# Kernel tuning notes

Hardware: AMD Instinct MI355X
Metric: run time of the kernel (lower is better)

The kernel has to match this reference:

```python
import jax, jax.numpy as jnp
import numpy as np

N = 100000      # nodes
E = 1600000     # edges (before self-loops)
IN_DIM = 128
HID = 32
HEADS = 4
OUT_DIM = 64
NEG_SLOPE = 0.2  # PyG GATConv default


def setup_inputs() -> dict:
    key = jax.random.key(0)
    ks = jax.random.split(key, 12)
    s1 = 1.0 / np.sqrt(IN_DIM).astype(np.float32)
    s2 = 1.0 / np.sqrt(HEADS * HID).astype(np.float32)
    return {
        "x": jax.random.normal(ks[0], (N, IN_DIM), jnp.float32),
        "edge_index": jax.random.randint(ks[1], (2, E), 0, N, dtype=jnp.int64),
        "W1": jax.random.normal(ks[2], (IN_DIM, HEADS * HID), jnp.float32) * s1,
        "att_src1": jax.random.normal(ks[3], (HEADS, HID), jnp.float32) * 0.1,
        "att_dst1": jax.random.normal(ks[4], (HEADS, HID), jnp.float32) * 0.1,
        "b1": jnp.zeros((HEADS * HID,), jnp.float32),
        "W2": jax.random.normal(ks[5], (HEADS * HID, OUT_DIM), jnp.float32) * s2,
        "att_src2": jax.random.normal(ks[6], (1, OUT_DIM), jnp.float32) * 0.1,
        "att_dst2": jax.random.normal(ks[7], (1, OUT_DIM), jnp.float32) * 0.1,
        "b2": jnp.zeros((OUT_DIM,), jnp.float32),
    }


def _gat_layer(x, src, dst, W, att_src, att_dst, bias, heads, out_ch, concat):
    # x: [N, F_in] -> h: [N, H, C]
    n = x.shape[0]
    h = (x @ W).reshape(n, heads, out_ch)
    # per-node attention logits, [N, H]
    a_src = jnp.einsum("nhc,hc->nh", h, att_src)
    a_dst = jnp.einsum("nhc,hc->nh", h, att_dst)
    # edge logits + LeakyReLU, [E, H]
    e = a_src[src] + a_dst[dst]
    e = jnp.where(e >= 0, e, NEG_SLOPE * e)
    # segment softmax over incoming edges of each dst node
    m = jax.ops.segment_max(e, dst, num_segments=n)          # [N, H]
    e = jnp.exp(e - m[dst])
    denom = jax.ops.segment_sum(e, dst, num_segments=n)      # [N, H]
    alpha = e / (denom[dst] + 1e-16)                          # [E, H]
    # weighted scatter-aggregate of source messages -> [N, H, C]
    out = jax.ops.segment_sum(h[src] * alpha[:, :, None], dst, num_segments=n)
    if concat:
        out = out.reshape(n, heads * out_ch)
    else:
        out = out.mean(axis=1)
    return out + bias


def reference(x, edge_index, W1, att_src1, att_dst1, b1, W2, att_src2, att_dst2, b2):
    n = x.shape[0]
    # PyG GATConv adds self-loops by default
    loops = jnp.arange(n, dtype=edge_index.dtype)
    src = jnp.concatenate([edge_index[0], loops])
    dst = jnp.concatenate([edge_index[1], loops])
    h = _gat_layer(x, src, dst, W1, att_src1, att_dst1, b1, HEADS, HID, concat=True)
    h = jax.nn.elu(h)
    # dropout p=0.5 is identity in eval mode (training=False)
    out = _gat_layer(h, src, dst, W2, att_src2, att_dst2, b2, 1, OUT_DIM, concat=False)
    return out
```

## Files before the change

### kernel.cpp

```cpp
#include <hip/hip_runtime.h>
#include <hip/hip_bf16.h>
#include <hip/hip_fp16.h>

#define NEG 0.2f
#define L2E 1.44269504f
#define BSH 9
#define BNODES 512
#define MAXC 16384
#define CHUNK 4096

typedef __attribute__((ext_vector_type(8))) _Float16 half8v;
typedef __attribute__((ext_vector_type(4))) short short4v;
typedef __attribute__((ext_vector_type(4))) float f32x4;

__device__ __forceinline__ float leaky(float e) { return fmaxf(e, NEG * e); }
__device__ __forceinline__ ushort f2h(float f) {
    __half h = __float2half(f);
    return *reinterpret_cast<ushort*>(&h);
}
__device__ __forceinline__ float edgep(float l, float adv, float e0) {
    return __builtin_amdgcn_exp2f(leaky(l + adv) - e0);
}

__device__ __forceinline__ void fma8(float* acc, float a, uint4 h) {
    unsigned wv[4] = { h.x, h.y, h.z, h.w };
    #pragma unroll
    for (int j = 0; j < 4; j++) {
        __half2 hh = *reinterpret_cast<__half2*>(&wv[j]);
        float lo = __half2float(__low2half(hh));
        float hi = __half2float(__high2half(hh));
        acc[2 * j]     = fmaf(a, lo, acc[2 * j]);
        acc[2 * j + 1] = fmaf(a, hi, acc[2 * j + 1]);
    }
}


__global__ __launch_bounds__(256) void k_bucket(const int* __restrict__ src, const int* __restrict__ dst,
                                                int E, unsigned int* __restrict__ bbuf,
                                                int* __restrict__ bcnt) {
    __shared__ int hcnt[256], hoff[256], gbase[256], sh[256];
    __shared__ unsigned int lbuf[CHUNK];
    __shared__ unsigned char map[CHUNK];
    int tid = threadIdx.x;
    hcnt[tid] = 0;
    __syncthreads();
    int e0 = blockIdx.x * CHUNK;
    unsigned int pk[16];
    int sl[16];
    unsigned char bb[16];
    #pragma unroll
    for (int r = 0; r < 16; r++) {
        int i = e0 + r * 256 + tid;
        sl[r] = -1; pk[r] = 0; bb[r] = 0;
        if (i < E) {
            int s = src[i], d = dst[i];
            int b = d >> BSH;
            pk[r] = ((unsigned int)(d & (BNODES - 1)) << 17) | (unsigned int)s;
            bb[r] = (unsigned char)b;
            sl[r] = atomicAdd(&hcnt[b], 1);
        }
    }
    __syncthreads();
    int v = hcnt[tid];
    sh[tid] = v;
    __syncthreads();
    for (int off = 1; off < 256; off <<= 1) {
        int t = (tid >= off) ? sh[tid - off] : 0;
        __syncthreads();
        sh[tid] += t;
        __syncthreads();
    }
    hoff[tid] = sh[tid] - v;
    if (v > 0) gbase[tid] = atomicAdd(&bcnt[tid], v);
    __syncthreads();
    #pragma unroll
    for (int r = 0; r < 16; r++) {
        if (sl[r] >= 0) {
            int pos = hoff[bb[r]] + sl[r];
            lbuf[pos] = pk[r];
            map[pos] = bb[r];
        }
    }
    int total = sh[255];
    __syncthreads();
    for (int j = tid; j < total; j += 256) {
        int lo = map[j];
        int p = gbase[lo] + (j - hoff[lo]);
        if (p < MAXC) bbuf[(size_t)lo * MAXC + p] = lbuf[j];
    }
}

__global__ void k_scanb(const int* __restrict__ bcnt, int nbuck, int* __restrict__ bbase) {
    __shared__ int sh[256];
    int tid = threadIdx.x;
    int v = (tid < nbuck) ? min(bcnt[tid], MAXC) : 0;
    sh[tid] = v;
    __syncthreads();
    for (int off = 1; off < 256; off <<= 1) {
        int t = (tid >= off) ? sh[tid - off] : 0;
        __syncthreads();
        sh[tid] += t;
        __syncthreads();
    }
    if (tid < nbuck) bbase[tid] = sh[tid] - v;
}

__global__ __launch_bounds__(256) void k_csrX(const unsigned int* __restrict__ bbuf,
                                              const int* __restrict__ bcnt, const int* __restrict__ bbase,
                                              int n, int E, int* __restrict__ rs, int* __restrict__ csr) {
    __shared__ int hist[BNODES], off[BNODES], cur[BNODES], sh[256];
    __shared__ unsigned int obuf[MAXC];
    int b = blockIdx.x, tid = threadIdx.x;
    hist[tid] = 0; hist[tid + 256] = 0;
    cur[tid] = 0;  cur[tid + 256] = 0;
    __syncthreads();
    int cnt = min(bcnt[b], MAXC);
    const unsigned int* p = bbuf + (size_t)b * MAXC;
    for (int i = tid; i < cnt; i += 256) atomicAdd(&hist[p[i] >> 17], 1);
    __syncthreads();
    int h0 = hist[2 * tid], h1v = hist[2 * tid + 1];
    int s = h0 + h1v;
    sh[tid] = s;
    __syncthreads();
    for (int o = 1; o < 256; o <<= 1) {
        int t = (tid >= o) ? sh[tid - o] : 0;
        __syncthreads();
        sh[tid] += t;
        __syncthreads();
    }
    int ex = sh[tid] - s;
    off[2 * tid] = ex;
    off[2 * tid + 1] = ex + h0;
    __syncthreads();
    int total = sh[255];
    int segbase = bbase[b];
    int n0 = b << BSH;
    for (int l = tid; l < BNODES; l += 256) {
        int node = n0 + l;
        if (node < n) rs[node] = segbase + off[l];
    }
    if (b == gridDim.x - 1 && tid == 0) rs[n] = segbase + total;
    for (int i = tid; i < cnt; i += 256) {
        unsigned int e = p[i];
        int l = e >> 17;
        int s2 = atomicAdd(&cur[l], 1);
        obuf[off[l] + s2] = e & 0x1FFFFu;
    }
    __syncthreads();
    for (int i = tid; i < cnt; i += 256) csr[segbase + i] = (int)obuf[i];
}

__global__ __launch_bounds__(256) void k_gemm1(const float* __restrict__ x, const float* __restrict__ W,
                                               const float* __restrict__ attS, const float* __restrict__ attD,
                                               ushort* __restrict__ h1b, float* __restrict__ as1,
                                               float* __restrict__ ad1, int n) {
    __shared__ ushort Wt[128 * 136];
    int tid = threadIdx.x;
    #pragma unroll 4
    for (int it = 0; it < 64; it++) {
        int idx = tid + 256 * it;
        int k = idx >> 7, nn = idx & 127;
        Wt[nn * 136 + k] = f2h(W[idx]);
    }
    __syncthreads();
    int lane = tid & 63;
    int wid = tid >> 6;
    int l15 = lane & 15, g = lane >> 4;
    int R0 = blockIdx.x * 128 + wid * 32;
    f32x4 acc[2][8];
    #pragma unroll
    for (int f = 0; f < 2; f++)
        #pragma unroll
        for (int nf = 0; nf < 8; nf++) acc[f][nf] = (f32x4){0.f, 0.f, 0.f, 0.f};
    size_t mclamp[2];
    mclamp[0] = (size_t)((R0 + l15 < n) ? R0 + l15 : n - 1);
    mclamp[1] = (size_t)((R0 + 16 + l15 < n) ? R0 + 16 + l15 : n - 1);
    #pragma unroll
    for (int ks = 0; ks < 4; ks++) {
        half8v xb[2];
        #pragma unroll
        for (int f = 0; f < 2; f++) {
            const float4* xp = (const float4*)(x + mclamp[f] * 128 + ks * 32 + g * 8);
            float4 a0 = xp[0], a1 = xp[1];
            half8v v;
            v[0] = (_Float16)a0.x; v[1] = (_Float16)a0.y; v[2] = (_Float16)a0.z; v[3] = (_Float16)a0.w;
            v[4] = (_Float16)a1.x; v[5] = (_Float16)a1.y; v[6] = (_Float16)a1.z; v[7] = (_Float16)a1.w;
            xb[f] = v;
        }
        #pragma unroll
        for (int nf = 0; nf < 8; nf++) {
            half8v wv = *(const half8v*)(&Wt[(16 * nf + l15) * 136 + ks * 32 + g * 8]);
            acc[0][nf] = __builtin_amdgcn_mfma_f32_16x16x32_f16(wv, xb[0], acc[0][nf], 0, 0, 0);
            acc[1][nf] = __builtin_amdgcn_mfma_f32_16x16x32_f16(wv, xb[1], acc[1][nf], 0, 0, 0);
        }
    }
    #pragma unroll
    for (int f = 0; f < 2; f++) {
        int m = R0 + 16 * f + l15;
        bool ok = m < n;
        float pS[4] = {0.f, 0.f, 0.f, 0.f}, pD[4] = {0.f, 0.f, 0.f, 0.f};
        #pragma unroll
        for (int nf = 0; nf < 8; nf++) {
            int n0 = 16 * nf + 4 * g;
            f32x4 a = acc[f][nf];
            if (ok) {
                short4v s4;
                s4[0] = (short)f2h(a[0]); s4[1] = (short)f2h(a[1]);
                s4[2] = (short)f2h(a[2]); s4[3] = (short)f2h(a[3]);
                *(short4v*)(h1b + (size_t)m * 128 + n0) = s4;
            }
            float4 vS = *(const float4*)(attS + n0);
            float4 vD = *(const float4*)(attD + n0);
            int hd = nf >> 1;
            pS[hd] += a[0] * vS.x + a[1] * vS.y + a[2] * vS.z + a[3] * vS.w;
            pD[hd] += a[0] * vD.x + a[1] * vD.y + a[2] * vD.z + a[3] * vD.w;
        }
        #pragma unroll
        for (int h = 0; h < 4; h++) {
            pS[h] += __shfl_xor(pS[h], 16, 64); pS[h] += __shfl_xor(pS[h], 32, 64);
            pD[h] += __shfl_xor(pD[h], 16, 64); pD[h] += __shfl_xor(pD[h], 32, 64);
        }
        if (ok && g == 0) {
            *(float4*)(as1 + (size_t)m * 4) = make_float4(pS[0] * L2E, pS[1] * L2E, pS[2] * L2E, pS[3] * L2E);
            *(float4*)(ad1 + (size_t)m * 4) = make_float4(pD[0] * L2E, pD[1] * L2E, pD[2] * L2E, pD[3] * L2E);
        }
    }
}

__global__ __launch_bounds__(256) void k_agg1(const int* __restrict__ rs, const int* __restrict__ csr,
                                              const ushort* __restrict__ h1b,
                                              const float* __restrict__ as1, const float* __restrict__ ad1,
                                              const float* __restrict__ b1,
                                              ushort* __restrict__ o1b, int n) {
    int w = (blockIdx.x * 256 + threadIdx.x) >> 6;
    w = __builtin_amdgcn_readfirstlane(w);
    if (w >= n) return;
    int lane = threadIdx.x & 63;
    int g = lane >> 4, q = lane & 15;
    int hd = q >> 2;
    unsigned qoff = 8u * (unsigned)q;
    float adv = ad1[(unsigned)(w * 4 + hd)];
    float e0 = leaky(as1[(unsigned)(w * 4 + hd)] + adv);
    float acc0[8], acc1[8];
    float den0 = 0.f, den1 = 0.f;
    #pragma unroll
    for (int c = 0; c < 8; c++) { acc0[c] = 0.f; acc1[c] = 0.f; }
    if (g == 0) {
        uint4 hv = *(const uint4*)(h1b + (((unsigned)w << 7) + qoff));
        fma8(acc0, 1.0f, hv);
        den0 = 1.0f;
    }
    int beg = rs[w], end = rs[w + 1];
    int i = beg;
    for (; i + 8 <= end; i += 8) {
        int ea = i + g, eb = i + 4 + g;
        int sa = csr[ea], sb = csr[eb];
        float pa = edgep(as1[(unsigned)(sa * 4 + hd)], adv, e0);
        float pb = edgep(as1[(unsigned)(sb * 4 + hd)], adv, e0);
        uint4 ha = *(const uint4*)(h1b + (((unsigned)sa << 7) + qoff));
        uint4 hb = *(const uint4*)(h1b + (((unsigned)sb << 7) + qoff));
        fma8(acc0, pa, ha);
        fma8(acc1, pb, hb);
        den0 += pa; den1 += pb;
    }
    if (i < end) {
        int ea = i + g;
        int ea2 = min(ea, end - 1);
        int sa = csr[ea2];
        float pa = (ea < end) ? edgep(as1[(unsigned)(sa * 4 + hd)], adv, e0) : 0.f;
        uint4 ha = *(const uint4*)(h1b + (((unsigned)sa << 7) + qoff));
        fma8(acc0, pa, ha);
        den0 += pa;
        if (i + 4 < end) {
            int eb = i + 4 + g;
            int eb2 = min(eb, end - 1);
            int sb = csr[eb2];
            float pb = (eb < end) ? edgep(as1[(unsigned)(sb * 4 + hd)], adv, e0) : 0.f;
            uint4 hb = *(const uint4*)(h1b + (((unsigned)sb << 7) + qoff));
            fma8(acc1, pb, hb);
            den1 += pb;
        }
    }
    float den = den0 + den1;
    den += __shfl_xor(den, 16, 64);
    den += __shfl_xor(den, 32, 64);
    #pragma unroll
    for (int c = 0; c < 8; c++) {
        float v = acc0[c] + acc1[c];
        v += __shfl_xor(v, 16, 64);
        v += __shfl_xor(v, 32, 64);
        acc0[c] = v;
    }
    if (g == 0) {
        float inv = 1.0f / den;
        float4 bv0 = *(const float4*)(b1 + 8 * q);
        float4 bv1 = *(const float4*)(b1 + 8 * q + 4);
        float o[8] = { acc0[0] * inv + bv0.x, acc0[1] * inv + bv0.y,
                       acc0[2] * inv + bv0.z, acc0[3] * inv + bv0.w,
                       acc0[4] * inv + bv1.x, acc0[5] * inv + bv1.y,
                       acc0[6] * inv + bv1.z, acc0[7] * inv + bv1.w };
        ushort st[8];
        #pragma unroll
        for (int c = 0; c < 8; c++) {
            float e = (o[c] > 0.f) ? o[c] : (__expf(o[c]) - 1.f);
            st[c] = f2h(e);
        }
        *(uint4*)(o1b + (((unsigned)w << 7) + qoff)) = *(uint4*)st;
    }
}

__global__ __launch_bounds__(256) void k_gemm2(const ushort* __restrict__ o1b, const float* __restrict__ W,
                                               const float* __restrict__ attS, const float* __restrict__ attD,
                                               ushort* __restrict__ h2b, float* __restrict__ as2,
                                               float* __restrict__ ad2, int n) {
    __shared__ ushort Wt[64 * 136];
    int tid = threadIdx.x;
    #pragma unroll 4
    for (int it = 0; it < 32; it++) {
        int idx = tid + 256 * it;
        int k = idx >> 6, nn = idx & 63;
        Wt[nn * 136 + k] = f2h(W[idx]);
    }
    __syncthreads();
    int lane = tid & 63;
    int wid = tid >> 6;
    int l15 = lane & 15, g = lane >> 4;
    int R0 = blockIdx.x * 128 + wid * 32;
    f32x4 acc[2][4];
    #pragma unroll
    for (int f = 0; f < 2; f++)
        #pragma unroll
        for (int nf = 0; nf < 4; nf++) acc[f][nf] = (f32x4){0.f, 0.f, 0.f, 0.f};
    size_t mclamp[2];
    mclamp[0] = (size_t)((R0 + l15 < n) ? R0 + l15 : n - 1);
    mclamp[1] = (size_t)((R0 + 16 + l15 < n) ? R0 + 16 + l15 : n - 1);
    #pragma unroll
    for (int ks = 0; ks < 4; ks++) {
        half8v xb[2];
        xb[0] = *(const half8v*)(o1b + mclamp[0] * 128 + ks * 32 + g * 8);
        xb[1] = *(const half8v*)(o1b + mclamp[1] * 128 + ks * 32 + g * 8);
        #pragma unroll
        for (int nf = 0; nf < 4; nf++) {
            half8v wv = *(const half8v*)(&Wt[(16 * nf + l15) * 136 + ks * 32 + g * 8]);
            acc[0][nf] = __builtin_amdgcn_mfma_f32_16x16x32_f16(wv, xb[0], acc[0][nf], 0, 0, 0);
            acc[1][nf] = __builtin_amdgcn_mfma_f32_16x16x32_f16(wv, xb[1], acc[1][nf], 0, 0, 0);
        }
    }
    #pragma unroll
    for (int f = 0; f < 2; f++) {
        int m = R0 + 16 * f + l15;
        bool ok = m < n;
        float pS = 0.f, pD = 0.f;
        #pragma unroll
        for (int nf = 0; nf < 4; nf++) {
            int n0 = 16 * nf + 4 * g;
            f32x4 a = acc[f][nf];
            if (ok) {
                short4v s4;
                s4[0] = (short)f2h(a[0]); s4[1] = (short)f2h(a[1]);
                s4[2] = (short)f2h(a[2]); s4[3] = (short)f2h(a[3]);
                *(short4v*)(h2b + (size_t)m * 64 + n0) = s4;
            }
            float4 vS = *(const float4*)(attS + n0);
            float4 vD = *(const float4*)(attD + n0);
            pS += a[0] * vS.x + a[1] * vS.y + a[2] * vS.z + a[3] * vS.w;
            pD += a[0] * vD.x + a[1] * vD.y + a[2] * vD.z + a[3] * vD.w;
        }
        pS += __shfl_xor(pS, 16, 64); pS += __shfl_xor(pS, 32, 64);
        pD += __shfl_xor(pD, 16, 64); pD += __shfl_xor(pD, 32, 64);
        if (ok && g == 0) {
            as2[m] = pS * L2E;
            ad2[m] = pD * L2E;
        }
    }
}

__global__ __launch_bounds__(256) void k_agg2(const int* __restrict__ rs, const int* __restrict__ csr,
                                              const ushort* __restrict__ h2b,
                                              const float* __restrict__ as2, const float* __restrict__ ad2,
                                              const float* __restrict__ b2,
                                              float* __restrict__ out, int n) {
    int w = (blockIdx.x * 256 + threadIdx.x) >> 6;
    w = __builtin_amdgcn_readfirstlane(w);
    if (w >= n) return;
    int lane = threadIdx.x & 63;
    int g = lane >> 3, q = lane & 7;
    unsigned qoff = 8u * (unsigned)q;
    float adv = ad2[w];
    float e0 = leaky(as2[w] + adv);
    float acc0[8], acc1[8];
    float den0 = 0.f, den1 = 0.f;
    #pragma unroll
    for (int c = 0; c < 8; c++) { acc0[c] = 0.f; acc1[c] = 0.f; }
    if (g == 0) {
        uint4 hv = *(const uint4*)(h2b + (((unsigned)w << 6) + qoff));
        fma8(acc0, 1.0f, hv);
        den0 = 1.0f;
    }
    int beg = rs[w], end = rs[w + 1];
    int i = beg;
    for (; i + 16 <= end; i += 16) {
        int ea = i + g, eb = i + 8 + g;
        int sa = csr[ea], sb = csr[eb];
        float pa = edgep(as2[(unsigned)sa], adv, e0);
        float pb = edgep(as2[(unsigned)sb], adv, e0);
        uint4 ha = *(const uint4*)(h2b + (((unsigned)sa << 6) + qoff));
        uint4 hb = *(const uint4*)(h2b + (((unsigned)sb << 6) + qoff));
        fma8(acc0, pa, ha);
        fma8(acc1, pb, hb);
        den0 += pa; den1 += pb;
    }
    for (; i < end; i += 8) {
        int e = i + g;
        int e2 = min(e, end - 1);
        int s = csr[e2];
        float p = (e < end) ? edgep(as2[(unsigned)s], adv, e0) : 0.f;
        uint4 hv = *(const uint4*)(h2b + (((unsigned)s << 6) + qoff));
        fma8(acc0, p, hv);
        den0 += p;
    }
    float den = den0 + den1;
    den += __shfl_xor(den, 8, 64);
    den += __shfl_xor(den, 16, 64);
    den += __shfl_xor(den, 32, 64);
    #pragma unroll
    for (int c = 0; c < 8; c++) {
        float v = acc0[c] + acc1[c];
        v += __shfl_xor(v, 8, 64);
        v += __shfl_xor(v, 16, 64);
        v += __shfl_xor(v, 32, 64);
        acc0[c] = v;
    }
    if (g == 0) {
        float inv = 1.0f / den;
        float4 bv0 = *(const float4*)(b2 + 8 * q);
        float4 bv1 = *(const float4*)(b2 + 8 * q + 4);
        float4 o0 = make_float4(acc0[0] * inv + bv0.x, acc0[1] * inv + bv0.y,
                                acc0[2] * inv + bv0.z, acc0[3] * inv + bv0.w);
        float4 o1 = make_float4(acc0[4] * inv + bv1.x, acc0[5] * inv + bv1.y,
                                acc0[6] * inv + bv1.z, acc0[7] * inv + bv1.w);
        *(float4*)(out + (size_t)w * 64 + 8 * q) = o0;
        *(float4*)(out + (size_t)w * 64 + 8 * q + 4) = o1;
    }
}

extern "C" void kernel_launch(void* const* d_in, const int* in_sizes, int n_in,
                              void* d_out, int out_size, void* d_ws, size_t ws_size,
                              hipStream_t stream) {
    const float* x     = (const float*)d_in[0];
    const int*   ei    = (const int*)d_in[1];
    const float* W1    = (const float*)d_in[2];
    const float* attS1 = (const float*)d_in[3];
    const float* attD1 = (const float*)d_in[4];
    const float* b1    = (const float*)d_in[5];
    const float* W2    = (const float*)d_in[6];
    const float* attS2 = (const float*)d_in[7];
    const float* attD2 = (const float*)d_in[8];
    const float* b2    = (const float*)d_in[9];
    float* out = (float*)d_out;

    int n = in_sizes[0] / 128;
    int E = in_sizes[1] / 2;
    const int* srcp = ei;
    const int* dstp = ei + E;
    int nbuck = (n + BNODES - 1) >> BSH;

    char* ws = (char*)d_ws;
    size_t off = 0;
    auto A = [&](size_t bytes) -> void* {
        void* p = ws + off;
        off = (off + bytes + 255) & ~(size_t)255;
        return p;
    };
    int* rs      = (int*)A((size_t)(n + 1) * 4);
    int* bcnt    = (int*)A(1024);
    int* bbase   = (int*)A(1024);
    int* csr     = (int*)A((size_t)E * 4);
    float* as1   = (float*)A((size_t)n * 16);
    float* ad1   = (float*)A((size_t)n * 16);
    float* as2   = (float*)A((size_t)n * 4);
    float* ad2   = (float*)A((size_t)n * 4);
    unsigned int* bbuf = (unsigned int*)A((size_t)nbuck * MAXC * 4);
    ushort* h1b  = (ushort*)A((size_t)n * 128 * 2);
    ushort* o1b  = (ushort*)A((size_t)n * 128 * 2);
    ushort* h2b  = h1b;

    hipMemsetAsync(bcnt, 0, 1024, stream);
    hipLaunchKernelGGL(k_bucket, dim3((E + CHUNK - 1) / CHUNK), dim3(256), 0, stream, srcp, dstp, E, bbuf, bcnt);
    hipLaunchKernelGGL(k_scanb, dim3(1), dim3(256), 0, stream, bcnt, nbuck, bbase);
    hipLaunchKernelGGL(k_csrX, dim3(nbuck), dim3(256), 0, stream, bbuf, bcnt, bbase, n, E, rs, csr);

    hipLaunchKernelGGL(k_gemm1, dim3((n + 127) / 128), dim3(256), 0, stream, x, W1, attS1, attD1, h1b, as1, ad1, n);
    hipLaunchKernelGGL(k_agg1, dim3((n * 64 + 255) / 256), dim3(256), 0, stream, rs, csr, h1b, as1, ad1, b1, o1b, n);
    hipLaunchKernelGGL(k_gemm2, dim3((n + 127) / 128), dim3(256), 0, stream, o1b, W2, attS2, attD2, h2b, as2, ad2, n);
    hipLaunchKernelGGL(k_agg2, dim3((n * 64 + 255) / 256), dim3(256), 0, stream, rs, csr, h2b, as2, ad2, b2, out, n);
}
```

Before: 216.6 us.

## Merge edge bucketing and first GEMM into one launch; shrink agg blocks

Fuses the edge-bucketing kernel and the layer-1 GEMM into a single heterogeneous launch. Block index selects the role, and both roles share one shared-memory buffer. The two stages are independent, so running them in one grid lets the memory-bound bucketing overlap the GEMM and removes one launch gap. The aggregation kernels also drop from 256-thread to 128-thread blocks for finer scheduling granularity. The cost is that the shared-memory footprint is now the larger of the two roles, which may limit occupancy for the bucketing blocks.

```diff
diff --git a/kernel.cpp b/kernel.cpp
--- a/kernel.cpp
+++ b/kernel.cpp
@@ -34,59 +34,139 @@
     }
 }
 
-
-__global__ __launch_bounds__(256) void k_bucket(const int* __restrict__ src, const int* __restrict__ dst,
-                                                int E, unsigned int* __restrict__ bbuf,
-                                                int* __restrict__ bcnt) {
-    __shared__ int hcnt[256], hoff[256], gbase[256], sh[256];
-    __shared__ unsigned int lbuf[CHUNK];
-    __shared__ unsigned char map[CHUNK];
+__global__ __launch_bounds__(256) void k_bktg1(const int* __restrict__ src, const int* __restrict__ dst,
+                                               int E, unsigned int* __restrict__ bbuf, int* __restrict__ bcnt,
+                                               int nbkt,
+                                               const float* __restrict__ x, const float* __restrict__ W,
+                                               const float* __restrict__ attS, const float* __restrict__ attD,
+                                               ushort* __restrict__ h1b, float* __restrict__ as1,
+                                               float* __restrict__ ad1, int n) {
+    __shared__ __align__(16) char smem[128 * 136 * 2];
     int tid = threadIdx.x;
-    hcnt[tid] = 0;
-    __syncthreads();
-    int e0 = blockIdx.x * CHUNK;
-    unsigned int pk[16];
-    int sl[16];
-    unsigned char bb[16];
-    #pragma unroll
-    for (int r = 0; r < 16; r++) {
-        int i = e0 + r * 256 + tid;
-        sl[r] = -1; pk[r] = 0; bb[r] = 0;
-        if (i < E) {
-            int s = src[i], d = dst[i];
-            int b = d >> BSH;
-            pk[r] = ((unsigned int)(d & (BNODES - 1)) << 17) | (unsigned int)s;
-            bb[r] = (unsigned char)b;
-            sl[r] = atomicAdd(&hcnt[b], 1);
-        }
-    }
-    __syncthreads();
-    int v = hcnt[tid];
-    sh[tid] = v;
-    __syncthreads();
-    for (int off = 1; off < 256; off <<= 1) {
-        int t = (tid >= off) ? sh[tid - off] : 0;
-        __syncthreads();
-        sh[tid] += t;
-        __syncthreads();
-    }
-    hoff[tid] = sh[tid] - v;
-    if (v > 0) gbase[tid] = atomicAdd(&bcnt[tid], v);
-    __syncthreads();
-    #pragma unroll
-    for (int r = 0; r < 16; r++) {
-        if (sl[r] >= 0) {
-            int pos = hoff[bb[r]] + sl[r];
-            lbuf[pos] = pk[r];
-            map[pos] = bb[r];
-        }
-    }
-    int total = sh[255];
-    __syncthreads();
-    for (int j = tid; j < total; j += 256) {
-        int lo = map[j];
-        int p = gbase[lo] + (j - hoff[lo]);
-        if (p < MAXC) bbuf[(size_t)lo * MAXC + p] = lbuf[j];
+    if (blockIdx.x < (unsigned)nbkt) {
+        int* hcnt = (int*)smem;
+        int* hoff = hcnt + 256;
+        int* gbase = hoff + 256;
+        int* sh = gbase + 256;
+        unsigned int* lbuf = (unsigned int*)(sh + 256);
+        unsigned char* map = (unsigned char*)(lbuf + CHUNK);
+        hcnt[tid] = 0;
+        __syncthreads();
+        int e0 = blockIdx.x * CHUNK;
+        unsigned int pk[16];
+        int sl[16];
+        unsigned char bb[16];
+        #pragma unroll
+        for (int r = 0; r < 16; r++) {
+            int i = e0 + r * 256 + tid;
+            sl[r] = -1; pk[r] = 0; bb[r] = 0;
+            if (i < E) {
+                int s = src[i], d = dst[i];
+                int b = d >> BSH;
+                pk[r] = ((unsigned int)(d & (BNODES - 1)) << 17) | (unsigned int)s;
+                bb[r] = (unsigned char)b;
+                sl[r] = atomicAdd(&hcnt[b], 1);
+            }
+        }
+        __syncthreads();
+        int v = hcnt[tid];
+        sh[tid] = v;
+        __syncthreads();
+        for (int off = 1; off < 256; off <<= 1) {
+            int t = (tid >= off) ? sh[tid - off] : 0;
+            __syncthreads();
+            sh[tid] += t;
+            __syncthreads();
+        }
+        hoff[tid] = sh[tid] - v;
+        if (v > 0) gbase[tid] = atomicAdd(&bcnt[tid], v);
+        __syncthreads();
+        #pragma unroll
+        for (int r = 0; r < 16; r++) {
+            if (sl[r] >= 0) {
+                int pos = hoff[bb[r]] + sl[r];
+                lbuf[pos] = pk[r];
+                map[pos] = bb[r];
+            }
+        }
+        int total = sh[255];
+        __syncthreads();
+        for (int j = tid; j < total; j += 256) {
+            int lo = map[j];
+            int p = gbase[lo] + (j - hoff[lo]);
+            if (p < MAXC) bbuf[(size_t)lo * MAXC + p] = lbuf[j];
+        }
+    } else {
+        ushort* Wt = (ushort*)smem;
+        #pragma unroll 4
+        for (int it = 0; it < 64; it++) {
+            int idx = tid + 256 * it;
+            int k = idx >> 7, nn = idx & 127;
+            Wt[nn * 136 + k] = f2h(W[idx]);
+        }
+        __syncthreads();
+        int lane = tid & 63;
+        int wid = tid >> 6;
+        int l15 = lane & 15, g = lane >> 4;
+        int R0 = (blockIdx.x - nbkt) * 128 + wid * 32;
+        f32x4 acc[2][8];
+        #pragma unroll
+        for (int f = 0; f < 2; f++)
+            #pragma unroll
+            for (int nf = 0; nf < 8; nf++) acc[f][nf] = (f32x4){0.f, 0.f, 0.f, 0.f};
+        size_t mclamp[2];
+        mclamp[0] = (size_t)((R0 + l15 < n) ? R0 + l15 : n - 1);
+        mclamp[1] = (size_t)((R0 + 16 + l15 < n) ? R0 + 16 + l15 : n - 1);
+        #pragma unroll
+        for (int ks = 0; ks < 4; ks++) {
+            half8v xb[2];
+            #pragma unroll
+            for (int f = 0; f < 2; f++) {
+                const float4* xp = (const float4*)(x + mclamp[f] * 128 + ks * 32 + g * 8);
+                float4 a0 = xp[0], a1 = xp[1];
+                half8v v;
+                v[0] = (_Float16)a0.x; v[1] = (_Float16)a0.y; v[2] = (_Float16)a0.z; v[3] = (_Float16)a0.w;
+                v[4] = (_Float16)a1.x; v[5] = (_Float16)a1.y; v[6] = (_Float16)a1.z; v[7] = (_Float16)a1.w;
+                xb[f] = v;
+            }
+            #pragma unroll
+            for (int nf = 0; nf < 8; nf++) {
+                half8v wv = *(const half8v*)(&Wt[(16 * nf + l15) * 136 + ks * 32 + g * 8]);
+                acc[0][nf] = __builtin_amdgcn_mfma_f32_16x16x32_f16(wv, xb[0], acc[0][nf], 0, 0, 0);
+                acc[1][nf] = __builtin_amdgcn_mfma_f32_16x16x32_f16(wv, xb[1], acc[1][nf], 0, 0, 0);
+            }
+        }
+        #pragma unroll
+        for (int f = 0; f < 2; f++) {
+            int m = R0 + 16 * f + l15;
+            bool ok = m < n;
+            float pS[4] = {0.f, 0.f, 0.f, 0.f}, pD[4] = {0.f, 0.f, 0.f, 0.f};
+            #pragma unroll
+            for (int nf = 0; nf < 8; nf++) {
+                int n0 = 16 * nf + 4 * g;
+                f32x4 a = acc[f][nf];
+                if (ok) {
+                    short4v s4;
+                    s4[0] = (short)f2h(a[0]); s4[1] = (short)f2h(a[1]);
+                    s4[2] = (short)f2h(a[2]); s4[3] = (short)f2h(a[3]);
+                    *(short4v*)(h1b + (size_t)m * 128 + n0) = s4;
+                }
+                float4 vS = *(const float4*)(attS + n0);
+                float4 vD = *(const float4*)(attD + n0);
+                int hd = nf >> 1;
+                pS[hd] += a[0] * vS.x + a[1] * vS.y + a[2] * vS.z + a[3] * vS.w;
+                pD[hd] += a[0] * vD.x + a[1] * vD.y + a[2] * vD.z + a[3] * vD.w;
+            }
+            #pragma unroll
+            for (int h = 0; h < 4; h++) {
+                pS[h] += __shfl_xor(pS[h], 16, 64); pS[h] += __shfl_xor(pS[h], 32, 64);
+                pD[h] += __shfl_xor(pD[h], 16, 64); pD[h] += __shfl_xor(pD[h], 32, 64);
+            }
+            if (ok && g == 0) {
+                *(float4*)(as1 + (size_t)m * 4) = make_float4(pS[0] * L2E, pS[1] * L2E, pS[2] * L2E, pS[3] * L2E);
+                *(float4*)(ad1 + (size_t)m * 4) = make_float4(pD[0] * L2E, pD[1] * L2E, pD[2] * L2E, pD[3] * L2E);
+            }
+        }
     }
 }
 
@@ -150,89 +230,12 @@
     for (int i = tid; i < cnt; i += 256) csr[segbase + i] = (int)obuf[i];
 }
 
-__global__ __launch_bounds__(256) void k_gemm1(const float* __restrict__ x, const float* __restrict__ W,
-                                               const float* __restrict__ attS, const float* __restrict__ attD,
-                                               ushort* __restrict__ h1b, float* __restrict__ as1,
-                                               float* __restrict__ ad1, int n) {
-    __shared__ ushort Wt[128 * 136];
-    int tid = threadIdx.x;
-    #pragma unroll 4
-    for (int it = 0; it < 64; it++) {
-        int idx = tid + 256 * it;
-        int k = idx >> 7, nn = idx & 127;
-        Wt[nn * 136 + k] = f2h(W[idx]);
-    }
-    __syncthreads();
-    int lane = tid & 63;
-    int wid = tid >> 6;
-    int l15 = lane & 15, g = lane >> 4;
-    int R0 = blockIdx.x * 128 + wid * 32;
-    f32x4 acc[2][8];
-    #pragma unroll
-    for (int f = 0; f < 2; f++)
-        #pragma unroll
-        for (int nf = 0; nf < 8; nf++) acc[f][nf] = (f32x4){0.f, 0.f, 0.f, 0.f};
-    size_t mclamp[2];
-    mclamp[0] = (size_t)((R0 + l15 < n) ? R0 + l15 : n - 1);
-    mclamp[1] = (size_t)((R0 + 16 + l15 < n) ? R0 + 16 + l15 : n - 1);
-    #pragma unroll
-    for (int ks = 0; ks < 4; ks++) {
-        half8v xb[2];
-        #pragma unroll
-        for (int f = 0; f < 2; f++) {
-            const float4* xp = (const float4*)(x + mclamp[f] * 128 + ks * 32 + g * 8);
-            float4 a0 = xp[0], a1 = xp[1];
-            half8v v;
-            v[0] = (_Float16)a0.x; v[1] = (_Float16)a0.y; v[2] = (_Float16)a0.z; v[3] = (_Float16)a0.w;
-            v[4] = (_Float16)a1.x; v[5] = (_Float16)a1.y; v[6] = (_Float16)a1.z; v[7] = (_Float16)a1.w;
-            xb[f] = v;
-        }
-        #pragma unroll
-        for (int nf = 0; nf < 8; nf++) {
-            half8v wv = *(const half8v*)(&Wt[(16 * nf + l15) * 136 + ks * 32 + g * 8]);
-            acc[0][nf] = __builtin_amdgcn_mfma_f32_16x16x32_f16(wv, xb[0], acc[0][nf], 0, 0, 0);
-            acc[1][nf] = __builtin_amdgcn_mfma_f32_16x16x32_f16(wv, xb[1], acc[1][nf], 0, 0, 0);
-        }
-    }
-    #pragma unroll
-    for (int f = 0; f < 2; f++) {
-        int m = R0 + 16 * f + l15;
-        bool ok = m < n;
-        float pS[4] = {0.f, 0.f, 0.f, 0.f}, pD[4] = {0.f, 0.f, 0.f, 0.f};
-        #pragma unroll
-        for (int nf = 0; nf < 8; nf++) {
-            int n0 = 16 * nf + 4 * g;
-            f32x4 a = acc[f][nf];
-            if (ok) {
-                short4v s4;
-                s4[0] = (short)f2h(a[0]); s4[1] = (short)f2h(a[1]);
-                s4[2] = (short)f2h(a[2]); s4[3] = (short)f2h(a[3]);
-                *(short4v*)(h1b + (size_t)m * 128 + n0) = s4;
-            }
-            float4 vS = *(const float4*)(attS + n0);
-            float4 vD = *(const float4*)(attD + n0);
-            int hd = nf >> 1;
-            pS[hd] += a[0] * vS.x + a[1] * vS.y + a[2] * vS.z + a[3] * vS.w;
-            pD[hd] += a[0] * vD.x + a[1] * vD.y + a[2] * vD.z + a[3] * vD.w;
-        }
-        #pragma unroll
-        for (int h = 0; h < 4; h++) {
-            pS[h] += __shfl_xor(pS[h], 16, 64); pS[h] += __shfl_xor(pS[h], 32, 64);
-            pD[h] += __shfl_xor(pD[h], 16, 64); pD[h] += __shfl_xor(pD[h], 32, 64);
-        }
-        if (ok && g == 0) {
-            *(float4*)(as1 + (size_t)m * 4) = make_float4(pS[0] * L2E, pS[1] * L2E, pS[2] * L2E, pS[3] * L2E);
-            *(float4*)(ad1 + (size_t)m * 4) = make_float4(pD[0] * L2E, pD[1] * L2E, pD[2] * L2E, pD[3] * L2E);
-        }
-    }
-}
-
-__global__ __launch_bounds__(256) void k_agg1(const int* __restrict__ rs, const int* __restrict__ csr,
+__global__ __launch_bounds__(128) void k_agg1(const int* __restrict__ rs, const int* __restrict__ csr,
                                               const ushort* __restrict__ h1b,
                                               const float* __restrict__ as1, const float* __restrict__ ad1,
                                               const float* __restrict__ b1,
                                               ushort* __restrict__ o1b, int n) {
-    int w = (blockIdx.x * 256 + threadIdx.x) >> 6;
+    int w = (blockIdx.x * 128 + threadIdx.x) >> 6;
     w = __builtin_amdgcn_readfirstlane(w);
     if (w >= n) return;
     int lane = threadIdx.x & 63;
@@ -375,12 +378,12 @@
     }
 }
 
-__global__ __launch_bounds__(256) void k_agg2(const int* __restrict__ rs, const int* __restrict__ csr,
+__global__ __launch_bounds__(128) void k_agg2(const int* __restrict__ rs, const int* __restrict__ csr,
                                               const ushort* __restrict__ h2b,
                                               const float* __restrict__ as2, const float* __restrict__ ad2,
                                               const float* __restrict__ b2,
                                               float* __restrict__ out, int n) {
-    int w = (blockIdx.x * 256 + threadIdx.x) >> 6;
+    int w = (blockIdx.x * 128 + threadIdx.x) >> 6;
     w = __builtin_amdgcn_readfirstlane(w);
     if (w >= n) return;
     int lane = threadIdx.x & 63;
@@ -464,6 +467,8 @@
     const int* srcp = ei;
     const int* dstp = ei + E;
     int nbuck = (n + BNODES - 1) >> BSH;
+    int nbkt = (E + CHUNK - 1) / CHUNK;
+    int ngemm1 = (n + 127) / 128;
 
     char* ws = (char*)d_ws;
     size_t off = 0;
@@ -486,12 +491,12 @@
     ushort* h2b  = h1b;
 
     hipMemsetAsync(bcnt, 0, 1024, stream);
-    hipLaunchKernelGGL(k_bucket, dim3((E + CHUNK - 1) / CHUNK), dim3(256), 0, stream, srcp, dstp, E, bbuf, bcnt);
+    hipLaunchKernelGGL(k_bktg1, dim3(nbkt + ngemm1), dim3(256), 0, stream,
+                       srcp, dstp, E, bbuf, bcnt, nbkt, x, W1, attS1, attD1, h1b, as1, ad1, n);
     hipLaunchKernelGGL(k_scanb, dim3(1), dim3(256), 0, stream, bcnt, nbuck, bbase);
     hipLaunchKernelGGL(k_csrX, dim3(nbuck), dim3(256), 0, stream, bbuf, bcnt, bbase, n, E, rs, csr);
 
-    hipLaunchKernelGGL(k_gemm1, dim3((n + 127) / 128), dim3(256), 0, stream, x, W1, attS1, attD1, h1b, as1, ad1, n);
-    hipLaunchKernelGGL(k_agg1, dim3((n * 64 + 255) / 256), dim3(256), 0, stream, rs, csr, h1b, as1, ad1, b1, o1b, n);
+    hipLaunchKernelGGL(k_agg1, dim3((n * 64 + 127) / 128), dim3(128), 0, stream, rs, csr, h1b, as1, ad1, b1, o1b, n);
     hipLaunchKernelGGL(k_gemm2, dim3((n + 127) / 128), dim3(256), 0, stream, o1b, W2, attS2, attD2, h2b, as2, ad2, n);
-    hipLaunchKernelGGL(k_agg2, dim3((n * 64 + 255) / 256), dim3(256), 0, stream, rs, csr, h2b, as2, ad2, b2, out, n);
-}
+    hipLaunchKernelGGL(k_agg2, dim3((n * 64 + 127) / 128), dim3(128), 0, stream, rs, csr, h2b, as2, ad2, b2, out, n);
+}
```

New measurement: 210.1 us. 1.03x faster.
